# Performance work log

Measured on AMD Instinct MI355X. Metric: run time of the kernel, lower is better.

Reference implementation:

```python
import jax, jax.numpy as jnp
import numpy as np

P0, P1 = 64, 4            # partition_size
NH, HD = 32, 16           # num_heads, head_dim
N = P0 * P1               # attn_area = tokens per window
B = 64                    # number of windows
C = 3 * NH * HD           # packed qkv channels


def _rel_index_1d(T):
    # relative_position_index from get_relative_position_index_1d
    idx = np.arange(T)
    return jnp.asarray(idx[:, None] - idx[None, :] + (T - 1))  # (T, T) in [0, 2T-2]


def setup_inputs() -> dict:
    key = jax.random.key(0)
    k1, k2 = jax.random.split(key)
    inp = jax.random.normal(k1, (B, N, C), dtype=jnp.float32)
    table = jax.random.normal(k2, (2 * P0 - 1, NH), dtype=jnp.float32) * 0.02
    return {"input": inp, "rel_bias_table": table}


def reference(input, rel_bias_table):
    Bq, Nq, Cq = input.shape
    hd = Cq // (3 * NH)
    # (B, N, 3, H, D) -> (3, B, H, N, D)
    qkv = input.reshape(Bq, Nq, 3, NH, hd).transpose(2, 0, 3, 1, 4)
    q, k, v = qkv[0], qkv[1], qkv[2]
    q = q * (NH ** -0.5)  # module scales by num_heads**-0.5 (as in source)
    attn = jnp.einsum('bhnd,bhmd->bhnm', q, k)  # (B, H, N, N)
    # type_1 relative positional bias: gather (P0,P0,H), tile over P1 on both axes
    rel_idx = _rel_index_1d(P0)
    bias = rel_bias_table[rel_idx]                       # (P0, P0, H)
    bias = jnp.broadcast_to(bias[:, None, :, None, :], (P0, P1, P0, P1, NH))
    bias = bias.reshape(N, N, NH).transpose(2, 0, 1)     # (H, N, N)
    attn = attn + bias[None]
    attn = jax.nn.softmax(attn, axis=-1)
    out = jnp.einsum('bhnm,bhmd->bhnd', attn, v)         # (B, H, N, D)
    return out.transpose(0, 2, 1, 3).reshape(Bq, Nq, NH * hd)
```

## Files before the change

### kernel.cpp

```cpp
#include <hip/hip_runtime.h>
#include <hip/hip_bf16.h>


typedef short bf16x8 __attribute__((ext_vector_type(8)));
typedef float f32x16 __attribute__((ext_vector_type(16)));

__device__ __forceinline__ unsigned int pk2(float a, float b) {
  __hip_bfloat162 hh = __float22bfloat162_rn(float2{a, b});
  unsigned int u; __builtin_memcpy(&u, &hh, 4); return u;
}

#if __has_builtin(__builtin_amdgcn_permlane32_swap)
typedef int i32x2_t __attribute__((ext_vector_type(2)));
__device__ __forceinline__ void swap_halves(unsigned x, unsigned y, unsigned& ox, unsigned& oy) {
  i32x2_t r = __builtin_amdgcn_permlane32_swap((int)x, (int)y, false, false);
  ox = (unsigned)r.x;
  oy = (unsigned)r.y;
}
#else
__device__ __forceinline__ void swap_halves(unsigned x, unsigned y, unsigned& ox, unsigned& oy) {
  const int hi = (threadIdx.x & 63) >> 5;
  unsigned tx = (unsigned)__shfl_xor((int)x, 32);
  unsigned ty = (unsigned)__shfl_xor((int)y, 32);
  ox = hi ? ty : x;
  oy = hi ? y : tx;
}
#endif

__global__ void mhsa_kernel(const float* __restrict__ inp, const float* __restrict__ table,
                            float* __restrict__ out) {
  const int bid = blockIdx.x;
  const int bh = ((bid & 7) << 8) | (bid >> 3);
  const int b = bh >> 5, h = bh & 31;
  const int t = threadIdx.x;
  const int l = t & 63;
  const int w = t >> 6;
  const int q32 = l & 31;
  const int hi = l >> 5;

  __shared__ __align__(16) short KF[8][64][8];
  __shared__ __align__(16) short VF[16][34][8];
  __shared__ float tbl[128];

  const float* gbase = inp + (size_t)b * (256 * 1536) + h * 16;
  const int row0 = t >> 2, c4 = t & 3;

  const float* p0 = gbase + (size_t)row0 * 1536 + c4 * 4;
  const float* p1 = gbase + (size_t)(row0 + 128) * 1536 + c4 * 4;
  float4 ka = *(const float4*)(p0 + 512);
  float4 va = *(const float4*)(p0 + 1024);
  float4 kb_ = *(const float4*)(p1 + 512);
  float4 vb_ = *(const float4*)(p1 + 1024);
  const float* qp = gbase + (size_t)(w * 32 + q32) * 1536 + hi * 8;
  float4 qa = *(const float4*)qp;
  float4 qb = *(const float4*)(qp + 4);

  if (t < 127) tbl[t] = table[t * 32 + h] * 1.4426950408889634f;
  if (t < 256) {
    const int kb = t >> 4, hv = (t >> 3) & 1, j = t & 7;
    VF[kb][hv * 17 + 16][j] = (short)0x3F80;
  }

  auto stage = [&](int row, const float4& kv, const float4& vv) {
    short* kdst = &KF[0][0][0] + (row >> 5) * 512 + ((c4 >> 1) * 32 + (row & 31)) * 8 + (c4 & 1) * 4;
    *(int2*)kdst = make_int2(pk2(kv.x, kv.y), pk2(kv.z, kv.w));
    unsigned v01 = pk2(vv.x, vv.y), v23 = pk2(vv.z, vv.w);
    short* vdst = &VF[0][0][0] + (row >> 4) * 272 + (((row >> 3) & 1) * 17 + c4 * 4) * 8 + (row & 7);
    vdst[0]  = (short)(v01 & 0xffff);
    vdst[8]  = (short)(v01 >> 16);
    vdst[16] = (short)(v23 & 0xffff);
    vdst[24] = (short)(v23 >> 16);
  };
  stage(row0, ka, va);
  stage(row0 + 128, kb_, vb_);

  bf16x8 q8;
  { unsigned qw[4] = { pk2(qa.x, qa.y), pk2(qa.z, qa.w),
                       pk2(qb.x, qb.y), pk2(qb.z, qb.w) };
    __builtin_memcpy(&q8, qw, 16); }

  __syncthreads();

  const float scale2 = 0.17677669529663687f * 1.4426950408889634f;
  const f32x16 z16 = {0.f};
  const short* kfb = &KF[0][0][0] + l * 8;
  const int vslot = hi * 17 + (q32 > 16 ? 16 : q32);
  const short* vfb = &VF[0][0][0] + vslot * 8;

  const int qbase = w * 32;
  const int bb = (qbase >> 2) + (q32 >> 2) + 63 - hi;

  auto body = [&](int kt, const f32x16& s, f32x16& o) {
    unsigned wd[8];
    #pragma unroll
    for (int m = 0; m < 4; ++m) {
      const float bias = tbl[bb - kt * 8 - 2 * m];
      float e0 = __builtin_amdgcn_exp2f(fmaf(s[4 * m + 0], scale2, bias));
      float e1 = __builtin_amdgcn_exp2f(fmaf(s[4 * m + 1], scale2, bias));
      float e2 = __builtin_amdgcn_exp2f(fmaf(s[4 * m + 2], scale2, bias));
      float e3 = __builtin_amdgcn_exp2f(fmaf(s[4 * m + 3], scale2, bias));
      wd[2 * m]     = pk2(e0, e1);
      wd[2 * m + 1] = pk2(e2, e3);
    }
    unsigned f0, f1, f2, f3;
    bf16x8 pf0, pf1;
    swap_halves(wd[0], wd[2], f0, f2);
    swap_halves(wd[1], wd[3], f1, f3);
    { unsigned a4[4] = { f0, f1, f2, f3 }; __builtin_memcpy(&pf0, a4, 16); }
    swap_halves(wd[4], wd[6], f0, f2);
    swap_halves(wd[5], wd[7], f1, f3);
    { unsigned a4[4] = { f0, f1, f2, f3 }; __builtin_memcpy(&pf1, a4, 16); }
    bf16x8 v0 = *(const bf16x8*)(vfb + (kt * 2 + 0) * 272);
    bf16x8 v1 = *(const bf16x8*)(vfb + (kt * 2 + 1) * 272);
    o = __builtin_amdgcn_mfma_f32_32x32x16_bf16(v0, pf0, o, 0, 0, 0);
    o = __builtin_amdgcn_mfma_f32_32x32x16_bf16(v1, pf1, o, 0, 0, 0);
  };

  f32x16 o = z16;
  {
    bf16x8 kf0 = *(const bf16x8*)kfb;
    f32x16 s = __builtin_amdgcn_mfma_f32_32x32x16_bf16(kf0, q8, z16, 0, 0, 0);
    #pragma unroll
    for (int kt = 0; kt < 7; ++kt) {
      bf16x8 kfn = *(const bf16x8*)(kfb + (kt + 1) * 512);
      f32x16 s_next = __builtin_amdgcn_mfma_f32_32x32x16_bf16(kfn, q8, z16, 0, 0, 0);
      body(kt, s, o);
      s = s_next;
    }
    body(7, s, o);
  }

  const float inv = 1.0f / __shfl(o[8], q32);
  float* op = out + (size_t)(b * 256 + qbase + q32) * 512 + h * 16 + hi * 4;
  float4 r0 = { o[0] * inv, o[1] * inv, o[2] * inv, o[3] * inv };
  float4 r1 = { o[4] * inv, o[5] * inv, o[6] * inv, o[7] * inv };
  *(float4*)op = r0;
  *(float4*)(op + 8) = r1;
}

extern "C" void kernel_launch(void* const* d_in, const int* in_sizes, int n_in,
                              void* d_out, int out_size, void* d_ws, size_t ws_size,
                              hipStream_t stream) {
  (void)in_sizes; (void)n_in; (void)out_size; (void)d_ws; (void)ws_size;
  const float* inp = (const float*)d_in[0];
  const float* tbl = (const float*)d_in[1];
  float* out = (float*)d_out;
  hipLaunchKernelGGL(mhsa_kernel, dim3(2048), dim3(512), 0, stream, inp, tbl, out);
}
```

Baseline: 36.03 us.

## Process four heads per block with async global-to-LDS prefetch of next K/V

Each block now loops over four consecutive (batch, head) pairs instead of one, cutting the grid from 2048 to 512 blocks. While the current head's attention runs, raw fp32 K/V for the next head are loaded straight into LDS with global_load_lds, and Q plus the bias table go into registers. The aim is to hide global load latency behind MFMA and exp work. The cost is fewer resident blocks, about 32KB more LDS per block, extra barriers, and the loss of the previous block-index swizzle.

```diff
diff --git a/kernel.cpp b/kernel.cpp
--- a/kernel.cpp
+++ b/kernel.cpp
@@ -27,66 +27,89 @@
 }
 #endif
 
+__device__ __forceinline__ void gload16(const float* g, float* lds_base, int lane) {
+#if __has_builtin(__builtin_amdgcn_global_load_lds)
+  const __attribute__((address_space(1))) unsigned int* gp =
+      reinterpret_cast<const __attribute__((address_space(1))) unsigned int*>(
+          reinterpret_cast<uintptr_t>(g));
+  __attribute__((address_space(3))) unsigned int* lp =
+      reinterpret_cast<__attribute__((address_space(3))) unsigned int*>(
+          reinterpret_cast<uintptr_t>(lds_base));
+  __builtin_amdgcn_global_load_lds(gp, lp, 16, 0, 0);
+#else
+  *(float4*)(lds_base + lane * 4) = *(const float4*)g;
+#endif
+}
+
 __global__ void mhsa_kernel(const float* __restrict__ inp, const float* __restrict__ table,
                             float* __restrict__ out) {
   const int bid = blockIdx.x;
-  const int bh = ((bid & 7) << 8) | (bid >> 3);
-  const int b = bh >> 5, h = bh & 31;
   const int t = threadIdx.x;
   const int l = t & 63;
   const int w = t >> 6;
   const int q32 = l & 31;
   const int hi = l >> 5;
+  const int bh0 = bid << 2;
 
   __shared__ __align__(16) short KF[8][64][8];
   __shared__ __align__(16) short VF[16][34][8];
   __shared__ float tbl[128];
+  __shared__ __align__(16) float Kraw[4096];
+  __shared__ __align__(16) float Vraw[4096];
 
-  const float* gbase = inp + (size_t)b * (256 * 1536) + h * 16;
-  const int row0 = t >> 2, c4 = t & 3;
-
-  const float* p0 = gbase + (size_t)row0 * 1536 + c4 * 4;
-  const float* p1 = gbase + (size_t)(row0 + 128) * 1536 + c4 * 4;
-  float4 ka = *(const float4*)(p0 + 512);
-  float4 va = *(const float4*)(p0 + 1024);
-  float4 kb_ = *(const float4*)(p1 + 512);
-  float4 vb_ = *(const float4*)(p1 + 1024);
-  const float* qp = gbase + (size_t)(w * 32 + q32) * 1536 + hi * 8;
-  float4 qa = *(const float4*)qp;
-  float4 qb = *(const float4*)(qp + 4);
-
-  if (t < 127) tbl[t] = table[t * 32 + h] * 1.4426950408889634f;
   if (t < 256) {
     const int kb = t >> 4, hv = (t >> 3) & 1, j = t & 7;
     VF[kb][hv * 17 + 16][j] = (short)0x3F80;
   }
 
-  auto stage = [&](int row, const float4& kv, const float4& vv) {
-    short* kdst = &KF[0][0][0] + (row >> 5) * 512 + ((c4 >> 1) * 32 + (row & 31)) * 8 + (c4 & 1) * 4;
-    *(int2*)kdst = make_int2(pk2(kv.x, kv.y), pk2(kv.z, kv.w));
-    unsigned v01 = pk2(vv.x, vv.y), v23 = pk2(vv.z, vv.w);
-    short* vdst = &VF[0][0][0] + (row >> 4) * 272 + (((row >> 3) & 1) * 17 + c4 * 4) * 8 + (row & 7);
-    vdst[0]  = (short)(v01 & 0xffff);
-    vdst[8]  = (short)(v01 >> 16);
-    vdst[16] = (short)(v23 & 0xffff);
-    vdst[24] = (short)(v23 >> 16);
+  const int lrow = l >> 2, lc4 = l & 3;
+
+  auto issue_raw = [&](int bh) {
+    const int b = bh >> 5, h = bh & 31;
+    const float* gb = inp + (size_t)b * 393216 + h * 16;
+    #pragma unroll
+    for (int j = 0; j < 2; ++j) {
+      const int rb = w * 32 + j * 16;
+      const float* gr = gb + (size_t)(rb + lrow) * 1536 + lc4 * 4;
+      gload16(gr + 512,  Kraw + rb * 16, l);
+      gload16(gr + 1024, Vraw + rb * 16, l);
+    }
   };
-  stage(row0, ka, va);
-  stage(row0 + 128, kb_, vb_);
 
-  bf16x8 q8;
-  { unsigned qw[4] = { pk2(qa.x, qa.y), pk2(qa.z, qa.w),
-                       pk2(qb.x, qb.y), pk2(qb.z, qb.w) };
-    __builtin_memcpy(&q8, qw, 16); }
+  float4 qa, qb; float tv;
+  auto issue_qt = [&](int bh) {
+    const int b = bh >> 5, h = bh & 31;
+    const float* qp = inp + (size_t)b * 393216 + h * 16
+                          + (size_t)(w * 32 + q32) * 1536 + hi * 8;
+    qa = *(const float4*)qp;
+    qb = *(const float4*)(qp + 4);
+    tv = (t < 127) ? table[t * 32 + h] : 0.f;
+  };
 
-  __syncthreads();
+  auto convert_frag = [&]() {
+    const int row0 = t >> 2, c4 = t & 3;
+    #pragma unroll
+    for (int rr = 0; rr < 2; ++rr) {
+      const int row = row0 + rr * 128;
+      const float4 kv = *(const float4*)(Kraw + row * 16 + c4 * 4);
+      const float4 vv = *(const float4*)(Vraw + row * 16 + c4 * 4);
+      short* kdst = &KF[0][0][0] + (row >> 5) * 512 + ((c4 >> 1) * 32 + (row & 31)) * 8 + (c4 & 1) * 4;
+      *(int2*)kdst = make_int2(pk2(kv.x, kv.y), pk2(kv.z, kv.w));
+      unsigned v01 = pk2(vv.x, vv.y), v23 = pk2(vv.z, vv.w);
+      short* vdst = &VF[0][0][0] + (row >> 4) * 272 + (((row >> 3) & 1) * 17 + c4 * 4) * 8 + (row & 7);
+      vdst[0]  = (short)(v01 & 0xffff);
+      vdst[8]  = (short)(v01 >> 16);
+      vdst[16] = (short)(v23 & 0xffff);
+      vdst[24] = (short)(v23 >> 16);
+    }
+    if (t < 127) tbl[t] = tv * 1.4426950408889634f;
+  };
 
   const float scale2 = 0.17677669529663687f * 1.4426950408889634f;
   const f32x16 z16 = {0.f};
   const short* kfb = &KF[0][0][0] + l * 8;
   const int vslot = hi * 17 + (q32 > 16 ? 16 : q32);
   const short* vfb = &VF[0][0][0] + vslot * 8;
-
   const int qbase = w * 32;
   const int bb = (qbase >> 2) + (q32 >> 2) + 63 - hi;
 
@@ -116,26 +139,46 @@
     o = __builtin_amdgcn_mfma_f32_32x32x16_bf16(v1, pf1, o, 0, 0, 0);
   };
 
-  f32x16 o = z16;
-  {
-    bf16x8 kf0 = *(const bf16x8*)kfb;
-    f32x16 s = __builtin_amdgcn_mfma_f32_32x32x16_bf16(kf0, q8, z16, 0, 0, 0);
-    #pragma unroll
-    for (int kt = 0; kt < 7; ++kt) {
-      bf16x8 kfn = *(const bf16x8*)(kfb + (kt + 1) * 512);
-      f32x16 s_next = __builtin_amdgcn_mfma_f32_32x32x16_bf16(kfn, q8, z16, 0, 0, 0);
-      body(kt, s, o);
-      s = s_next;
+  issue_raw(bh0);
+  issue_qt(bh0);
+  __syncthreads();
+
+  #pragma unroll 1
+  for (int i = 0; i < 4; ++i) {
+    convert_frag();
+    bf16x8 q8;
+    { unsigned qw[4] = { pk2(qa.x, qa.y), pk2(qa.z, qa.w),
+                         pk2(qb.x, qb.y), pk2(qb.z, qb.w) };
+      __builtin_memcpy(&q8, qw, 16); }
+    __syncthreads();
+
+    if (i < 3) { issue_raw(bh0 + i + 1); issue_qt(bh0 + i + 1); }
+
+    f32x16 o = z16;
+    {
+      bf16x8 kf0 = *(const bf16x8*)kfb;
+      f32x16 s = __builtin_amdgcn_mfma_f32_32x32x16_bf16(kf0, q8, z16, 0, 0, 0);
+      #pragma unroll
+      for (int kt = 0; kt < 7; ++kt) {
+        bf16x8 kfn = *(const bf16x8*)(kfb + (kt + 1) * 512);
+        f32x16 s_next = __builtin_amdgcn_mfma_f32_32x32x16_bf16(kfn, q8, z16, 0, 0, 0);
+        body(kt, s, o);
+        s = s_next;
+      }
+      body(7, s, o);
     }
-    body(7, s, o);
+
+    const int bh = bh0 + i;
+    const int b = bh >> 5, h = bh & 31;
+    const float inv = 1.0f / __shfl(o[8], q32);
+    float* op = out + (size_t)(b * 256 + qbase + q32) * 512 + h * 16 + hi * 4;
+    float4 r0 = { o[0] * inv, o[1] * inv, o[2] * inv, o[3] * inv };
+    float4 r1 = { o[4] * inv, o[5] * inv, o[6] * inv, o[7] * inv };
+    *(float4*)op = r0;
+    *(float4*)(op + 8) = r1;
+
+    if (i < 3) __syncthreads();
   }
-
-  const float inv = 1.0f / __shfl(o[8], q32);
-  float* op = out + (size_t)(b * 256 + qbase + q32) * 512 + h * 16 + hi * 4;
-  float4 r0 = { o[0] * inv, o[1] * inv, o[2] * inv, o[3] * inv };
-  float4 r1 = { o[4] * inv, o[5] * inv, o[6] * inv, o[7] * inv };
-  *(float4*)op = r0;
-  *(float4*)(op + 8) = r1;
 }
 
 extern "C" void kernel_launch(void* const* d_in, const int* in_sizes, int n_in,
@@ -145,5 +188,5 @@
   const float* inp = (const float*)d_in[0];
   const float* tbl = (const float*)d_in[1];
   float* out = (float*)d_out;
-  hipLaunchKernelGGL(mhsa_kernel, dim3(2048), dim3(512), 0, stream, inp, tbl, out);
+  hipLaunchKernelGGL(mhsa_kernel, dim3(512), dim3(512), 0, stream, inp, tbl, out);
 }
```

After: 48.98 us. 36.0% more time.
